# Performance work log

Hardware: AMD Instinct MI355X
Metric: run time of the kernel (lower is better)

Reference implementation:

```python
import jax, jax.numpy as jnp
import numpy as np

HEADS = 8
DIM_HEAD = 64


def setup_inputs() -> dict:
    key = jax.random.key(0)
    ks = jax.random.split(key, 4)
    B, C, H, W = 1, 256, 64, 64
    inner = HEADS * DIM_HEAD  # 512
    x = jax.random.normal(ks[0], (B, C, H, W), dtype=jnp.float32)
    norm_w = jnp.ones((C,), dtype=jnp.float32)                      # RMSNorm weight (1,C,1,1) flattened
    w_qkv = jax.random.normal(ks[1], (3 * inner, C), dtype=jnp.float32) * 0.02  # 1x1 conv, no bias
    w_out = jax.random.normal(ks[2], (C, inner), dtype=jnp.float32) * 0.02      # 1x1 conv
    b_out = jax.random.normal(ks[3], (C,), dtype=jnp.float32) * 0.02
    return {"x": x, "norm_w": norm_w, "w_qkv": w_qkv, "w_out": w_out, "b_out": b_out}


def reference(x, norm_w, w_qkv, w_out, b_out):
    B, C, H, W = x.shape
    N = H * W
    # RMSNorm: F.normalize over channel dim (L2, eps clamp) * weight * sqrt(C)
    l2 = jnp.sqrt(jnp.sum(x * x, axis=1, keepdims=True))
    xn = x / jnp.maximum(l2, 1e-12) * norm_w[None, :, None, None] * (C ** 0.5)
    # 1x1 conv QKV = channel matmul
    qkv = jnp.einsum('oc,bchw->bohw', w_qkv, xn)  # [B, 3*inner, H, W]
    q, k, v = jnp.split(qkv, 3, axis=1)

    def split_heads(t):
        # 'b (h d) x y -> b h (x y) d'
        return t.reshape(B, HEADS, DIM_HEAD, N).transpose(0, 1, 3, 2)

    q, k, v = map(split_heads, (q, k, v))
    scale = DIM_HEAD ** -0.5
    scores = jnp.einsum('bhnd,bhmd->bhnm', q, k) * scale  # [B,H,N,N]
    attn = jax.nn.softmax(scores, axis=-1)
    out = jnp.einsum('bhnm,bhmd->bhnd', attn, v)
    # 'b h (x y) d -> b (h d) x y'
    out = out.transpose(0, 1, 3, 2).reshape(B, HEADS * DIM_HEAD, H, W)
    # output 1x1 conv + residual (note: residual is the NORMALIZED x, per source)
    return jnp.einsum('ci,bihw->bchw', w_out, out) + b_out[None, :, None, None] + xn
```

## Files before the change

kernel.cpp:

```cpp
#include <hip/hip_runtime.h>


#define NPIX 4096
#define CIN 256
#define INNER 512
#define NHEAD 8
#define DH 64

typedef __bf16 bf16;
typedef __attribute__((ext_vector_type(8))) __bf16 bf16x8;
typedef __attribute__((ext_vector_type(4))) float f32x4;

static __device__ __forceinline__ f32x4 mfma_bf16(bf16x8 a, bf16x8 b, f32x4 c) {
  return __builtin_amdgcn_mfma_f32_16x16x32_bf16(a, b, c, 0, 0, 0);
}

static __device__ __forceinline__ unsigned pack_bf16x2(float lo, float hi) {
  unsigned short a = __builtin_bit_cast(unsigned short, (bf16)lo);
  unsigned short b = __builtin_bit_cast(unsigned short, (bf16)hi);
  return (unsigned)a | ((unsigned)b << 16);
}

__global__ __launch_bounds__(256) void k_cvt(const float* __restrict__ a,
                                             bf16* __restrict__ b, int n) {
  int i = blockIdx.x * 256 + threadIdx.x;
  if (i < n) b[i] = (bf16)a[i];
}

__global__ __launch_bounds__(256) void k_rmsnorm(const float* __restrict__ x,
                                                 const float* __restrict__ w,
                                                 float* __restrict__ xn,
                                                 bf16* __restrict__ xnT) {
  const int wave = threadIdx.x >> 6, lane = threadIdx.x & 63;
  const int p = blockIdx.x * 64 + lane;
  __shared__ float red[4][64];
  float ss = 0.f;
  for (int i = 0; i < 64; ++i) {
    float v = x[(wave * 64 + i) * NPIX + p];
    ss += v * v;
  }
  red[wave][lane] = ss;
  __syncthreads();
  float tot = red[0][lane] + red[1][lane] + red[2][lane] + red[3][lane];
  float inv = 16.0f / fmaxf(sqrtf(tot), 1e-12f);
  for (int i = 0; i < 64; ++i) {
    int c = wave * 64 + i;
    float v = x[c * NPIX + p] * inv * w[c];
    xn[c * NPIX + p] = v;
    xnT[p * CIN + c] = (bf16)v;
  }
}

__global__ __launch_bounds__(256) void k_qkv(const bf16* __restrict__ wqkv,
                                             const bf16* __restrict__ xnT,
                                             bf16* __restrict__ qT,
                                             bf16* __restrict__ kT,
                                             bf16* __restrict__ vv) {
  const int lane = threadIdx.x & 63, wave = threadIdx.x >> 6;
  const int l15 = lane & 15, quad = lane >> 4;
  const int obase = blockIdx.y * 64 + (wave >> 1) * 32;
  const int pbase = blockIdx.x * 128 + (wave & 1) * 64;
  const int sect = blockIdx.y >> 3;
  f32x4 acc[8];
#pragma unroll
  for (int i = 0; i < 8; ++i) acc[i] = (f32x4){0.f, 0.f, 0.f, 0.f};
#pragma unroll
  for (int kc = 0; kc < CIN / 32; ++kc) {
    bf16x8 af[2], bfr[4];
#pragma unroll
    for (int oc = 0; oc < 2; ++oc)
      af[oc] = *(const bf16x8*)(wqkv + (size_t)(obase + oc * 16 + l15) * CIN + kc * 32 + quad * 8);
#pragma unroll
    for (int pc = 0; pc < 4; ++pc)
      bfr[pc] = *(const bf16x8*)(xnT + (size_t)(pbase + pc * 16 + l15) * CIN + kc * 32 + quad * 8);
    if (sect < 2) {
#pragma unroll
      for (int pc = 0; pc < 4; ++pc)
#pragma unroll
        for (int oc = 0; oc < 2; ++oc)
          acc[pc * 2 + oc] = mfma_bf16(bfr[pc], af[oc], acc[pc * 2 + oc]);
    } else {
#pragma unroll
      for (int oc = 0; oc < 2; ++oc)
#pragma unroll
        for (int pc = 0; pc < 4; ++pc)
          acc[oc * 4 + pc] = mfma_bf16(af[oc], bfr[pc], acc[oc * 4 + pc]);
    }
  }
  if (sect < 2) {
    bf16* dst = (sect == 0) ? qT : kT;
    const int head = blockIdx.y & 7;
    const int dd = (wave >> 1) * 32;
#pragma unroll
    for (int pc = 0; pc < 4; ++pc)
#pragma unroll
      for (int oc = 0; oc < 2; ++oc)
#pragma unroll
        for (int r = 0; r < 4; ++r) {
          int p = pbase + pc * 16 + quad * 4 + r;
          dst[((size_t)(head << 12) + p) * DH + dd + oc * 16 + l15] =
              (bf16)acc[pc * 2 + oc][r];
        }
  } else {
#pragma unroll
    for (int oc = 0; oc < 2; ++oc)
#pragma unroll
      for (int r = 0; r < 4; ++r) {
        int o = obase + oc * 16 + quad * 4 + r - 2 * INNER;
#pragma unroll
        for (int pc = 0; pc < 4; ++pc)
          vv[(size_t)o * NPIX + pbase + pc * 16 + l15] = (bf16)acc[oc * 4 + pc][r];
      }
  }
}

__global__ __launch_bounds__(256, 2) void k_attn(const bf16* __restrict__ qT,
                                                 const bf16* __restrict__ kT,
                                                 const bf16* __restrict__ vv,
                                                 bf16* __restrict__ Ows) {
  const int head = blockIdx.y;
  const int tid = threadIdx.x;
  const int wave = tid >> 6, lane = tid & 63;
  const int l15 = lane & 15, quad = lane >> 4;
  const int qb = blockIdx.x * 64;

  __shared__ float Om[4][4][64][17];
  __shared__ float Ll[4][4][16];

  bf16x8 qf[4][2];
#pragma unroll
  for (int qt = 0; qt < 4; ++qt)
#pragma unroll
    for (int kc = 0; kc < 2; ++kc)
      qf[qt][kc] = *(const bf16x8*)(qT + ((size_t)(head << 12) + qb + qt * 16 + l15) * DH + kc * 32 + quad * 8);

  f32x4 o[4][4];
#pragma unroll
  for (int qt = 0; qt < 4; ++qt)
#pragma unroll
    for (int c = 0; c < 4; ++c) o[qt][c] = (f32x4){0.f, 0.f, 0.f, 0.f};
  float lsum[4] = {0.f, 0.f, 0.f, 0.f};

  const bf16* kbase = kT + (size_t)(head << 12) * DH;
  const bf16* vbase = vv + (size_t)(head * DH) * NPIX;
  const int kb0 = wave * (NPIX / 4);
  const int srcA = ((quad & 1) << 5) + l15;
  const int srcB = srcA + 16;
  const float SC = 0.18033688f;

  bf16x8 kf[2][2], kfn[2][2];
#pragma unroll
  for (int nc = 0; nc < 2; ++nc)
#pragma unroll
    for (int kc = 0; kc < 2; ++kc)
      kf[nc][kc] = *(const bf16x8*)(kbase + (size_t)(kb0 + nc * 16 + l15) * DH + kc * 32 + quad * 8);

  for (int it = 0; it < 32; ++it) {
    const int kb = kb0 + it * 32;
    bf16x8 vf[4];
#pragma unroll
    for (int c = 0; c < 4; ++c)
      vf[c] = *(const bf16x8*)(vbase + (size_t)(c * 16 + l15) * NPIX + kb + quad * 8);
    const int kbn = kb0 + ((it + 1) & 31) * 32;
#pragma unroll
    for (int nc = 0; nc < 2; ++nc)
#pragma unroll
      for (int kc = 0; kc < 2; ++kc)
        kfn[nc][kc] = *(const bf16x8*)(kbase + (size_t)(kbn + nc * 16 + l15) * DH + kc * 32 + quad * 8);

    f32x4 s[4][2];
#pragma unroll
    for (int qt = 0; qt < 4; ++qt)
#pragma unroll
      for (int nc = 0; nc < 2; ++nc) {
        s[qt][nc] = mfma_bf16(kf[nc][0], qf[qt][0], (f32x4){0.f, 0.f, 0.f, 0.f});
        s[qt][nc] = mfma_bf16(kf[nc][1], qf[qt][1], s[qt][nc]);
      }

#pragma unroll
    for (int qt = 0; qt < 4; ++qt) {
      unsigned pk[4];
#pragma unroll
      for (int r = 0; r < 4; ++r) {
        float p0 = exp2f(s[qt][0][r] * SC);
        float p1 = exp2f(s[qt][1][r] * SC);
        lsum[qt] += p0 + p1;
        pk[r] = pack_bf16x2(p0, p1);
      }
      union { bf16x8 v; unsigned short u[8]; } pf;
#pragma unroll
      for (int j = 0; j < 4; ++j) {
        unsigned w0 = (unsigned)__shfl((int)pk[j], srcA);
        unsigned w1 = (unsigned)__shfl((int)pk[j], srcB);
        pf.u[j] = (unsigned short)(quad < 2 ? w0 : (w0 >> 16));
        pf.u[j + 4] = (unsigned short)(quad < 2 ? w1 : (w1 >> 16));
      }
#pragma unroll
      for (int c = 0; c < 4; ++c) o[qt][c] = mfma_bf16(vf[c], pf.v, o[qt][c]);
    }

#pragma unroll
    for (int nc = 0; nc < 2; ++nc)
#pragma unroll
      for (int kc = 0; kc < 2; ++kc) kf[nc][kc] = kfn[nc][kc];
  }

#pragma unroll
  for (int qt = 0; qt < 4; ++qt) {
    float ls = lsum[qt];
    ls += __shfl_xor(ls, 16);
    ls += __shfl_xor(ls, 32);
    if (quad == 0) Ll[wave][qt][l15] = ls;
#pragma unroll
    for (int c = 0; c < 4; ++c)
#pragma unroll
      for (int r = 0; r < 4; ++r)
        Om[wave][qt][c * 16 + quad * 4 + r][l15] = o[qt][c][r];
  }
  __syncthreads();

  const int d = tid & 63;
  const int qg = tid >> 6;
#pragma unroll
  for (int qt = 0; qt < 4; ++qt)
#pragma unroll
    for (int i = 0; i < 4; ++i) {
      int q = qg * 4 + i;
      float O = Om[0][qt][d][q] + Om[1][qt][d][q] + Om[2][qt][d][q] + Om[3][qt][d][q];
      float L = Ll[0][qt][q] + Ll[1][qt][q] + Ll[2][qt][q] + Ll[3][qt][q];
      Ows[((size_t)(head << 12) + qb + qt * 16 + q) * DH + d] = (bf16)(O / L);
    }
}

__global__ __launch_bounds__(256) void k_oproj(const bf16* __restrict__ wout,
                                               const bf16* __restrict__ Ows,
                                               const float* __restrict__ bout,
                                               const float* __restrict__ xn,
                                               float* __restrict__ out) {
  const int lane = threadIdx.x & 63, wave = threadIdx.x >> 6;
  const int l15 = lane & 15, quad = lane >> 4;
  const int mbase = blockIdx.y * 32 + (wave >> 1) * 16;
  const int pbase = blockIdx.x * 64 + (wave & 1) * 32;
  f32x4 acc[2];
  acc[0] = (f32x4){0.f, 0.f, 0.f, 0.f};
  acc[1] = (f32x4){0.f, 0.f, 0.f, 0.f};
#pragma unroll
  for (int kc = 0; kc < INNER / 32; ++kc) {
    bf16x8 af = *(const bf16x8*)(wout + (size_t)(mbase + l15) * INNER + kc * 32 + quad * 8);
    int i0 = kc * 32 + quad * 8;
    int head = i0 >> 6, d0 = i0 & 63;
#pragma unroll
    for (int pc = 0; pc < 2; ++pc) {
      bf16x8 bfr = *(const bf16x8*)(Ows + ((size_t)(head << 12) + pbase + pc * 16 + l15) * DH + d0);
      acc[pc] = mfma_bf16(af, bfr, acc[pc]);
    }
  }
#pragma unroll
  for (int pc = 0; pc < 2; ++pc)
#pragma unroll
    for (int r = 0; r < 4; ++r) {
      int c = mbase + quad * 4 + r, p = pbase + pc * 16 + l15;
      out[c * NPIX + p] = acc[pc][r] + bout[c] + xn[c * NPIX + p];
    }
}

extern "C" void kernel_launch(void* const* d_in, const int* in_sizes, int n_in,
                              void* d_out, int out_size, void* d_ws, size_t ws_size,
                              hipStream_t stream) {
  (void)in_sizes; (void)n_in; (void)out_size; (void)ws_size;
  const float* x      = (const float*)d_in[0];
  const float* norm_w = (const float*)d_in[1];
  const float* w_qkv  = (const float*)d_in[2];
  const float* w_out  = (const float*)d_in[3];
  const float* b_out  = (const float*)d_in[4];
  float* out = (float*)d_out;

  char* ws = (char*)d_ws;
  float* xn    = (float*)(ws);
  bf16* xnT    = (bf16*)(ws + (4u << 20));
  bf16* qT     = (bf16*)(ws + (6u << 20));
  bf16* kT     = (bf16*)(ws + (10u << 20));
  bf16* vv     = (bf16*)(ws + (14u << 20));
  bf16* Ows    = (bf16*)(ws + (18u << 20));
  bf16* wqkv_b = (bf16*)(ws + (22u << 20));
  bf16* wout_b = (bf16*)(ws + (23u << 20));

  hipLaunchKernelGGL(k_cvt, dim3((3 * INNER * CIN + 255) / 256), dim3(256), 0, stream,
                     w_qkv, wqkv_b, 3 * INNER * CIN);
  hipLaunchKernelGGL(k_cvt, dim3((CIN * INNER + 255) / 256), dim3(256), 0, stream,
                     w_out, wout_b, CIN * INNER);
  hipLaunchKernelGGL(k_rmsnorm, dim3(NPIX / 64), dim3(256), 0, stream, x, norm_w, xn, xnT);
  hipLaunchKernelGGL(k_qkv, dim3(NPIX / 128, 1536 / 64), dim3(256), 0, stream,
                     wqkv_b, xnT, qT, kT, vv);
  hipLaunchKernelGGL(k_attn, dim3(NPIX / 64, NHEAD), dim3(256), 0, stream,
                     qT, kT, vv, Ows);
  hipLaunchKernelGGL(k_oproj, dim3(NPIX / 64, CIN / 32), dim3(256), 0, stream,
                     wout_b, Ows, b_out, xn, out);
}
```

Before: 183.5 us.

## Switch to fp16 MFMA, fold softmax scale into Q, MFMA row sums

Converts every intermediate and MFMA from bf16 to fp16. The softmax scale and log2e are folded into Q when it is written, so the attention loop calls the raw exp2 builtin with no multiply. Probabilities are packed with cvt_pkrtz and fewer shuffles. Row sums come from an extra MFMA against a ones vector instead of scalar adds and cross-lane reductions. The RMSNorm kernel is also retiled to 16 pixels per block, giving more blocks. The attention loop still does no max subtraction, so fp16 overflow of exp values is a new accuracy risk.

```diff
diff --git a/kernel.cpp b/kernel.cpp
--- a/kernel.cpp
+++ b/kernel.cpp
@@ -7,55 +7,55 @@
 #define NHEAD 8
 #define DH 64
 
-typedef __bf16 bf16;
-typedef __attribute__((ext_vector_type(8))) __bf16 bf16x8;
+typedef _Float16 f16;
+typedef __attribute__((ext_vector_type(8))) _Float16 f16x8;
 typedef __attribute__((ext_vector_type(4))) float f32x4;
 
-static __device__ __forceinline__ f32x4 mfma_bf16(bf16x8 a, bf16x8 b, f32x4 c) {
-  return __builtin_amdgcn_mfma_f32_16x16x32_bf16(a, b, c, 0, 0, 0);
-}
-
-static __device__ __forceinline__ unsigned pack_bf16x2(float lo, float hi) {
-  unsigned short a = __builtin_bit_cast(unsigned short, (bf16)lo);
-  unsigned short b = __builtin_bit_cast(unsigned short, (bf16)hi);
-  return (unsigned)a | ((unsigned)b << 16);
+static __device__ __forceinline__ f32x4 mfma_f16(f16x8 a, f16x8 b, f32x4 c) {
+  return __builtin_amdgcn_mfma_f32_16x16x32_f16(a, b, c, 0, 0, 0);
+}
+
+static __device__ __forceinline__ unsigned pk2(float lo, float hi) {
+  return __builtin_bit_cast(unsigned, __builtin_amdgcn_cvt_pkrtz(lo, hi));
 }
 
 __global__ __launch_bounds__(256) void k_cvt(const float* __restrict__ a,
-                                             bf16* __restrict__ b, int n) {
+                                             f16* __restrict__ b, int n) {
   int i = blockIdx.x * 256 + threadIdx.x;
-  if (i < n) b[i] = (bf16)a[i];
+  if (i < n) b[i] = (f16)a[i];
 }
 
 __global__ __launch_bounds__(256) void k_rmsnorm(const float* __restrict__ x,
                                                  const float* __restrict__ w,
                                                  float* __restrict__ xn,
-                                                 bf16* __restrict__ xnT) {
-  const int wave = threadIdx.x >> 6, lane = threadIdx.x & 63;
-  const int p = blockIdx.x * 64 + lane;
-  __shared__ float red[4][64];
+                                                 f16* __restrict__ xnT) {
+  const int pi = threadIdx.x & 15, cs = threadIdx.x >> 4;
+  const int p = blockIdx.x * 16 + pi;
+  __shared__ float red[16][16];
   float ss = 0.f;
-  for (int i = 0; i < 64; ++i) {
-    float v = x[(wave * 64 + i) * NPIX + p];
+  for (int i = 0; i < 16; ++i) {
+    float v = x[(cs * 16 + i) * NPIX + p];
     ss += v * v;
   }
-  red[wave][lane] = ss;
+  red[cs][pi] = ss;
   __syncthreads();
-  float tot = red[0][lane] + red[1][lane] + red[2][lane] + red[3][lane];
+  float tot = 0.f;
+#pragma unroll
+  for (int s = 0; s < 16; ++s) tot += red[s][pi];
   float inv = 16.0f / fmaxf(sqrtf(tot), 1e-12f);
-  for (int i = 0; i < 64; ++i) {
-    int c = wave * 64 + i;
+  for (int i = 0; i < 16; ++i) {
+    int c = cs * 16 + i;
     float v = x[c * NPIX + p] * inv * w[c];
     xn[c * NPIX + p] = v;
-    xnT[p * CIN + c] = (bf16)v;
-  }
-}
-
-__global__ __launch_bounds__(256) void k_qkv(const bf16* __restrict__ wqkv,
-                                             const bf16* __restrict__ xnT,
-                                             bf16* __restrict__ qT,
-                                             bf16* __restrict__ kT,
-                                             bf16* __restrict__ vv) {
+    xnT[p * CIN + c] = (f16)v;
+  }
+}
+
+__global__ __launch_bounds__(256) void k_qkv(const f16* __restrict__ wqkv,
+                                             const f16* __restrict__ xnT,
+                                             f16* __restrict__ qT,
+                                             f16* __restrict__ kT,
+                                             f16* __restrict__ vv) {
   const int lane = threadIdx.x & 63, wave = threadIdx.x >> 6;
   const int l15 = lane & 15, quad = lane >> 4;
   const int obase = blockIdx.y * 64 + (wave >> 1) * 32;
@@ -66,29 +66,30 @@
   for (int i = 0; i < 8; ++i) acc[i] = (f32x4){0.f, 0.f, 0.f, 0.f};
 #pragma unroll
   for (int kc = 0; kc < CIN / 32; ++kc) {
-    bf16x8 af[2], bfr[4];
+    f16x8 af[2], bfr[4];
 #pragma unroll
     for (int oc = 0; oc < 2; ++oc)
-      af[oc] = *(const bf16x8*)(wqkv + (size_t)(obase + oc * 16 + l15) * CIN + kc * 32 + quad * 8);
+      af[oc] = *(const f16x8*)(wqkv + (size_t)(obase + oc * 16 + l15) * CIN + kc * 32 + quad * 8);
 #pragma unroll
     for (int pc = 0; pc < 4; ++pc)
-      bfr[pc] = *(const bf16x8*)(xnT + (size_t)(pbase + pc * 16 + l15) * CIN + kc * 32 + quad * 8);
+      bfr[pc] = *(const f16x8*)(xnT + (size_t)(pbase + pc * 16 + l15) * CIN + kc * 32 + quad * 8);
     if (sect < 2) {
 #pragma unroll
       for (int pc = 0; pc < 4; ++pc)
 #pragma unroll
         for (int oc = 0; oc < 2; ++oc)
-          acc[pc * 2 + oc] = mfma_bf16(bfr[pc], af[oc], acc[pc * 2 + oc]);
+          acc[pc * 2 + oc] = mfma_f16(bfr[pc], af[oc], acc[pc * 2 + oc]);
     } else {
 #pragma unroll
       for (int oc = 0; oc < 2; ++oc)
 #pragma unroll
         for (int pc = 0; pc < 4; ++pc)
-          acc[oc * 4 + pc] = mfma_bf16(af[oc], bfr[pc], acc[oc * 4 + pc]);
+          acc[oc * 4 + pc] = mfma_f16(af[oc], bfr[pc], acc[oc * 4 + pc]);
     }
   }
   if (sect < 2) {
-    bf16* dst = (sect == 0) ? qT : kT;
+    f16* dst = (sect == 0) ? qT : kT;
+    const float sc = (sect == 0) ? 0.18033688f : 1.0f;
     const int head = blockIdx.y & 7;
     const int dd = (wave >> 1) * 32;
 #pragma unroll
@@ -99,7 +100,7 @@
         for (int r = 0; r < 4; ++r) {
           int p = pbase + pc * 16 + quad * 4 + r;
           dst[((size_t)(head << 12) + p) * DH + dd + oc * 16 + l15] =
-              (bf16)acc[pc * 2 + oc][r];
+              (f16)(acc[pc * 2 + oc][r] * sc);
         }
   } else {
 #pragma unroll
@@ -109,15 +110,15 @@
         int o = obase + oc * 16 + quad * 4 + r - 2 * INNER;
 #pragma unroll
         for (int pc = 0; pc < 4; ++pc)
-          vv[(size_t)o * NPIX + pbase + pc * 16 + l15] = (bf16)acc[oc * 4 + pc][r];
+          vv[(size_t)o * NPIX + pbase + pc * 16 + l15] = (f16)acc[oc * 4 + pc][r];
       }
   }
 }
 
-__global__ __launch_bounds__(256, 2) void k_attn(const bf16* __restrict__ qT,
-                                                 const bf16* __restrict__ kT,
-                                                 const bf16* __restrict__ vv,
-                                                 bf16* __restrict__ Ows) {
+__global__ __launch_bounds__(256, 2) void k_attn(const f16* __restrict__ qT,
+                                                 const f16* __restrict__ kT,
+                                                 const f16* __restrict__ vv,
+                                                 f16* __restrict__ Ows) {
   const int head = blockIdx.y;
   const int tid = threadIdx.x;
   const int wave = tid >> 6, lane = tid & 63;
@@ -127,76 +128,78 @@
   __shared__ float Om[4][4][64][17];
   __shared__ float Ll[4][4][16];
 
-  bf16x8 qf[4][2];
+  f16x8 qf[4][2];
 #pragma unroll
   for (int qt = 0; qt < 4; ++qt)
 #pragma unroll
     for (int kc = 0; kc < 2; ++kc)
-      qf[qt][kc] = *(const bf16x8*)(qT + ((size_t)(head << 12) + qb + qt * 16 + l15) * DH + kc * 32 + quad * 8);
-
-  f32x4 o[4][4];
-#pragma unroll
-  for (int qt = 0; qt < 4; ++qt)
+      qf[qt][kc] = *(const f16x8*)(qT + ((size_t)(head << 12) + qb + qt * 16 + l15) * DH + kc * 32 + quad * 8);
+
+  f32x4 o[4][4], ol[4];
+#pragma unroll
+  for (int qt = 0; qt < 4; ++qt) {
 #pragma unroll
     for (int c = 0; c < 4; ++c) o[qt][c] = (f32x4){0.f, 0.f, 0.f, 0.f};
-  float lsum[4] = {0.f, 0.f, 0.f, 0.f};
-
-  const bf16* kbase = kT + (size_t)(head << 12) * DH;
-  const bf16* vbase = vv + (size_t)(head * DH) * NPIX;
+    ol[qt] = (f32x4){0.f, 0.f, 0.f, 0.f};
+  }
+
+  const f16* kbase = kT + (size_t)(head << 12) * DH;
+  const f16* vbase = vv + (size_t)(head * DH) * NPIX;
   const int kb0 = wave * (NPIX / 4);
   const int srcA = ((quad & 1) << 5) + l15;
   const int srcB = srcA + 16;
-  const float SC = 0.18033688f;
-
-  bf16x8 kf[2][2], kfn[2][2];
+  const bool hiQuad = quad >= 2;
+  const f16x8 onesv = {1.f16, 1.f16, 1.f16, 1.f16, 1.f16, 1.f16, 1.f16, 1.f16};
+
+  f16x8 kf[2][2], kfn[2][2];
 #pragma unroll
   for (int nc = 0; nc < 2; ++nc)
 #pragma unroll
     for (int kc = 0; kc < 2; ++kc)
-      kf[nc][kc] = *(const bf16x8*)(kbase + (size_t)(kb0 + nc * 16 + l15) * DH + kc * 32 + quad * 8);
+      kf[nc][kc] = *(const f16x8*)(kbase + (size_t)(kb0 + nc * 16 + l15) * DH + kc * 32 + quad * 8);
 
   for (int it = 0; it < 32; ++it) {
     const int kb = kb0 + it * 32;
-    bf16x8 vf[4];
+    f16x8 vf[4];
 #pragma unroll
     for (int c = 0; c < 4; ++c)
-      vf[c] = *(const bf16x8*)(vbase + (size_t)(c * 16 + l15) * NPIX + kb + quad * 8);
+      vf[c] = *(const f16x8*)(vbase + (size_t)(c * 16 + l15) * NPIX + kb + quad * 8);
     const int kbn = kb0 + ((it + 1) & 31) * 32;
 #pragma unroll
     for (int nc = 0; nc < 2; ++nc)
 #pragma unroll
       for (int kc = 0; kc < 2; ++kc)
-        kfn[nc][kc] = *(const bf16x8*)(kbase + (size_t)(kbn + nc * 16 + l15) * DH + kc * 32 + quad * 8);
+        kfn[nc][kc] = *(const f16x8*)(kbase + (size_t)(kbn + nc * 16 + l15) * DH + kc * 32 + quad * 8);
 
     f32x4 s[4][2];
 #pragma unroll
     for (int qt = 0; qt < 4; ++qt)
 #pragma unroll
       for (int nc = 0; nc < 2; ++nc) {
-        s[qt][nc] = mfma_bf16(kf[nc][0], qf[qt][0], (f32x4){0.f, 0.f, 0.f, 0.f});
-        s[qt][nc] = mfma_bf16(kf[nc][1], qf[qt][1], s[qt][nc]);
+        s[qt][nc] = mfma_f16(kf[nc][0], qf[qt][0], (f32x4){0.f, 0.f, 0.f, 0.f});
+        s[qt][nc] = mfma_f16(kf[nc][1], qf[qt][1], s[qt][nc]);
       }
 
 #pragma unroll
     for (int qt = 0; qt < 4; ++qt) {
-      unsigned pk[4];
+      float p0[4], p1[4];
 #pragma unroll
       for (int r = 0; r < 4; ++r) {
-        float p0 = exp2f(s[qt][0][r] * SC);
-        float p1 = exp2f(s[qt][1][r] * SC);
-        lsum[qt] += p0 + p1;
-        pk[r] = pack_bf16x2(p0, p1);
+        p0[r] = __builtin_amdgcn_exp2f(s[qt][0][r]);
+        p1[r] = __builtin_amdgcn_exp2f(s[qt][1][r]);
       }
-      union { bf16x8 v; unsigned short u[8]; } pf;
-#pragma unroll
-      for (int j = 0; j < 4; ++j) {
-        unsigned w0 = (unsigned)__shfl((int)pk[j], srcA);
-        unsigned w1 = (unsigned)__shfl((int)pk[j], srcB);
-        pf.u[j] = (unsigned short)(quad < 2 ? w0 : (w0 >> 16));
-        pf.u[j + 4] = (unsigned short)(quad < 2 ? w1 : (w1 >> 16));
-      }
-#pragma unroll
-      for (int c = 0; c < 4; ++c) o[qt][c] = mfma_bf16(vf[c], pf.v, o[qt][c]);
+      unsigned A0 = pk2(p0[0], p0[1]), B0 = pk2(p0[2], p0[3]);
+      unsigned A1 = pk2(p1[0], p1[1]), B1 = pk2(p1[2], p1[3]);
+      unsigned As = hiQuad ? A1 : A0;
+      unsigned Bs = hiQuad ? B1 : B0;
+      union { f16x8 v; unsigned u[4]; } pf;
+      pf.u[0] = (unsigned)__shfl((int)As, srcA);
+      pf.u[1] = (unsigned)__shfl((int)Bs, srcA);
+      pf.u[2] = (unsigned)__shfl((int)As, srcB);
+      pf.u[3] = (unsigned)__shfl((int)Bs, srcB);
+#pragma unroll
+      for (int c = 0; c < 4; ++c) o[qt][c] = mfma_f16(vf[c], pf.v, o[qt][c]);
+      ol[qt] = mfma_f16(onesv, pf.v, ol[qt]);
     }
 
 #pragma unroll
@@ -207,10 +210,7 @@
 
 #pragma unroll
   for (int qt = 0; qt < 4; ++qt) {
-    float ls = lsum[qt];
-    ls += __shfl_xor(ls, 16);
-    ls += __shfl_xor(ls, 32);
-    if (quad == 0) Ll[wave][qt][l15] = ls;
+    if (quad == 0) Ll[wave][qt][l15] = ol[qt][0];
 #pragma unroll
     for (int c = 0; c < 4; ++c)
 #pragma unroll
@@ -228,12 +228,12 @@
       int q = qg * 4 + i;
       float O = Om[0][qt][d][q] + Om[1][qt][d][q] + Om[2][qt][d][q] + Om[3][qt][d][q];
       float L = Ll[0][qt][q] + Ll[1][qt][q] + Ll[2][qt][q] + Ll[3][qt][q];
-      Ows[((size_t)(head << 12) + qb + qt * 16 + q) * DH + d] = (bf16)(O / L);
-    }
-}
-
-__global__ __launch_bounds__(256) void k_oproj(const bf16* __restrict__ wout,
-                                               const bf16* __restrict__ Ows,
+      Ows[((size_t)(head << 12) + qb + qt * 16 + q) * DH + d] = (f16)(O / L);
+    }
+}
+
+__global__ __launch_bounds__(256) void k_oproj(const f16* __restrict__ wout,
+                                               const f16* __restrict__ Ows,
                                                const float* __restrict__ bout,
                                                const float* __restrict__ xn,
                                                float* __restrict__ out) {
@@ -246,13 +246,13 @@
   acc[1] = (f32x4){0.f, 0.f, 0.f, 0.f};
 #pragma unroll
   for (int kc = 0; kc < INNER / 32; ++kc) {
-    bf16x8 af = *(const bf16x8*)(wout + (size_t)(mbase + l15) * INNER + kc * 32 + quad * 8);
+    f16x8 af = *(const f16x8*)(wout + (size_t)(mbase + l15) * INNER + kc * 32 + quad * 8);
     int i0 = kc * 32 + quad * 8;
     int head = i0 >> 6, d0 = i0 & 63;
 #pragma unroll
     for (int pc = 0; pc < 2; ++pc) {
-      bf16x8 bfr = *(const bf16x8*)(Ows + ((size_t)(head << 12) + pbase + pc * 16 + l15) * DH + d0);
-      acc[pc] = mfma_bf16(af, bfr, acc[pc]);
+      f16x8 bfr = *(const f16x8*)(Ows + ((size_t)(head << 12) + pbase + pc * 16 + l15) * DH + d0);
+      acc[pc] = mfma_f16(af, bfr, acc[pc]);
     }
   }
 #pragma unroll
@@ -277,23 +277,23 @@
 
   char* ws = (char*)d_ws;
   float* xn    = (float*)(ws);
-  bf16* xnT    = (bf16*)(ws + (4u << 20));
-  bf16* qT     = (bf16*)(ws + (6u << 20));
-  bf16* kT     = (bf16*)(ws + (10u << 20));
-  bf16* vv     = (bf16*)(ws + (14u << 20));
-  bf16* Ows    = (bf16*)(ws + (18u << 20));
-  bf16* wqkv_b = (bf16*)(ws + (22u << 20));
-  bf16* wout_b = (bf16*)(ws + (23u << 20));
+  f16* xnT     = (f16*)(ws + (4u << 20));
+  f16* qT      = (f16*)(ws + (6u << 20));
+  f16* kT      = (f16*)(ws + (10u << 20));
+  f16* vv      = (f16*)(ws + (14u << 20));
+  f16* Ows     = (f16*)(ws + (18u << 20));
+  f16* wqkv_h  = (f16*)(ws + (22u << 20));
+  f16* wout_h  = (f16*)(ws + (23u << 20));
 
   hipLaunchKernelGGL(k_cvt, dim3((3 * INNER * CIN + 255) / 256), dim3(256), 0, stream,
-                     w_qkv, wqkv_b, 3 * INNER * CIN);
+                     w_qkv, wqkv_h, 3 * INNER * CIN);
   hipLaunchKernelGGL(k_cvt, dim3((CIN * INNER + 255) / 256), dim3(256), 0, stream,
-                     w_out, wout_b, CIN * INNER);
-  hipLaunchKernelGGL(k_rmsnorm, dim3(NPIX / 64), dim3(256), 0, stream, x, norm_w, xn, xnT);
+                     w_out, wout_h, CIN * INNER);
+  hipLaunchKernelGGL(k_rmsnorm, dim3(NPIX / 16), dim3(256), 0, stream, x, norm_w, xn, xnT);
   hipLaunchKernelGGL(k_qkv, dim3(NPIX / 128, 1536 / 64), dim3(256), 0, stream,
-                     wqkv_b, xnT, qT, kT, vv);
+                     wqkv_h, xnT, qT, kT, vv);
   hipLaunchKernelGGL(k_attn, dim3(NPIX / 64, NHEAD), dim3(256), 0, stream,
                      qT, kT, vv, Ows);
   hipLaunchKernelGGL(k_oproj, dim3(NPIX / 64, CIN / 32), dim3(256), 0, stream,
-                     wout_b, Ows, b_out, xn, out);
-}
+                     wout_h, Ows, b_out, xn, out);
+}
```

Result: faster. 168.4 us (-8.2%).
